# Optimization experiments

Hardware: AMD Instinct MI355X
Metric: run time of the kernel (lower is better)

Reference implementation:

```python
import jax, jax.numpy as jnp
import numpy as np

NUM_HEADS = 16
BLOCK = 64  # block_size = min(64, N)

def setup_inputs() -> dict:
    key = jax.random.key(0)
    k0, k1, k2 = jax.random.split(key, 3)
    B, N, C = 2, 2048, 1024
    x = jax.random.normal(k0, (B, N, C), dtype=jnp.float32)
    w_qkv = jax.random.normal(k1, (3 * C, C), dtype=jnp.float32) * 0.02  # torch Linear weight [out,in]
    w_proj = jax.random.normal(k2, (C, C), dtype=jnp.float32) * 0.02
    b_proj = jnp.zeros((C,), dtype=jnp.float32)
    return {"x": x, "w_qkv": w_qkv, "w_proj": w_proj, "b_proj": b_proj}

def reference(x, w_qkv, w_proj, b_proj):
    B, N, C = x.shape
    H = NUM_HEADS
    hd = C // H
    bs = min(BLOCK, N)
    scale = hd ** -0.5
    # qkv projection: [B,N,3C] -> [3,B,H,N,hd]
    qkv = (x @ w_qkv.T).reshape(B, N, 3, H, hd).transpose(2, 0, 3, 1, 4)
    q, k, v = qkv[0], qkv[1], qkv[2]
    # block-causal mask: query block i attends to all key blocks <= i
    blk = jnp.arange(N) // bs
    mask = blk[:, None] >= blk[None, :]  # [N,N]
    scores = jnp.einsum('bhqd,bhkd->bhqk', q, k) * scale
    scores = jnp.where(mask, scores, -jnp.inf)
    weights = jax.nn.softmax(scores, axis=-1)
    out = jnp.einsum('bhqk,bhkd->bhqd', weights, v)
    out = out.transpose(0, 2, 1, 3).reshape(B, N, C)
    return out @ w_proj.T + b_proj
```

## Files before the change

### kernel.cpp

```cpp
#include <hip/hip_runtime.h>

typedef __attribute__((ext_vector_type(8))) short bf16x8;
typedef __attribute__((ext_vector_type(4))) float f32x4;
typedef __attribute__((ext_vector_type(2))) unsigned int u32x2;

__device__ __forceinline__ unsigned short f2bf(float f) {
  unsigned int u = __float_as_uint(f);
  u += 0x7fffu + ((u >> 16) & 1u);
  return (unsigned short)(u >> 16);
}

__device__ __forceinline__ void gload_lds16(const unsigned short* g, unsigned short* l) {
  __builtin_amdgcn_global_load_lds(
      (const __attribute__((address_space(1))) unsigned int*)g,
      (__attribute__((address_space(3))) unsigned int*)l,
      16, 0, 0);
}

__global__ void cvt_all(const float* __restrict__ x, const float* __restrict__ wq,
                        const float* __restrict__ wp, unsigned short* __restrict__ dst) {
  const int n1 = 4096 * 1024 / 4, n2 = 3072 * 1024 / 4, n3 = 1024 * 1024 / 4;
  int stride = gridDim.x * blockDim.x;
  for (int i = blockIdx.x * blockDim.x + threadIdx.x; i < n1 + n2 + n3; i += stride) {
    const float* s; int j;
    if (i < n1)           { s = x;  j = i; }
    else if (i < n1 + n2) { s = wq; j = i - n1; }
    else                  { s = wp; j = i - n1 - n2; }
    float4 v = ((const float4*)s)[j];
    ushort4 o;
    o.x = f2bf(v.x); o.y = f2bf(v.y); o.z = f2bf(v.z); o.w = f2bf(v.w);
    ((ushort4*)dst)[i] = o;
  }
}

__device__ __forceinline__ void gemm128_bt(const unsigned short* __restrict__ A,
                                           const unsigned short* __restrict__ Bt,
                                           unsigned short* As, unsigned short* Bs,
                                           int tm, int tn, f32x4 acc[4][4]) {
  const int K = 1024;
  int tid = threadIdx.x;
  int w = tid >> 6, l = tid & 63;
  int wr = w >> 1, wc = w & 1;
  int g = l >> 4, c = l & 15;

  int srow = w * 32 + (l >> 2);
  int skoff = (((l & 3) ^ ((srow >> 1) & 3)) * 8);
  const unsigned short* gA = A + (size_t)(tm * 128 + srow) * K + skoff;
  const unsigned short* gB = Bt + (size_t)(tn * 128 + srow) * K + skoff;
  unsigned short* lA = As + (w * 32) * 32;
  unsigned short* lB = Bs + (w * 32) * 32;

  int rx = (c >> 1) & 3;
  int arow = wr * 64 + c;
  int brow = wc * 64 + c;

  for (int k0 = 0; k0 < K; k0 += 32) {
    gload_lds16(gA, lA);
    gload_lds16(gA + 16 * K, lA + 16 * 32);
    gload_lds16(gB, lB);
    gload_lds16(gB + 16 * K, lB + 16 * 32);
    gA += 32; gB += 32;
    __syncthreads();
    bf16x8 af[4], bfr[4];
#pragma unroll
    for (int mi = 0; mi < 4; ++mi)
      af[mi] = *(const bf16x8*)((const char*)As + (arow + mi * 16) * 64 + ((g ^ rx) << 4));
#pragma unroll
    for (int ni = 0; ni < 4; ++ni)
      bfr[ni] = *(const bf16x8*)((const char*)Bs + (brow + ni * 16) * 64 + ((g ^ rx) << 4));
#pragma unroll
    for (int mi = 0; mi < 4; ++mi)
#pragma unroll
      for (int ni = 0; ni < 4; ++ni)
        acc[mi][ni] = __builtin_amdgcn_mfma_f32_16x16x32_bf16(af[mi], bfr[ni], acc[mi][ni], 0, 0, 0);
    __syncthreads();
  }
}

__global__ __launch_bounds__(256) void qkv_gemm(const unsigned short* __restrict__ xb,
                                                const unsigned short* __restrict__ wb,
                                                unsigned short* __restrict__ Qp,
                                                unsigned short* __restrict__ Kp,
                                                unsigned short* __restrict__ Vt) {
  __shared__ unsigned short As[128 * 32];
  __shared__ unsigned short Bs[128 * 32];
  f32x4 acc[4][4];
#pragma unroll
  for (int i = 0; i < 4; ++i)
#pragma unroll
    for (int j = 0; j < 4; ++j) acc[i][j] = f32x4{0.f, 0.f, 0.f, 0.f};
  int id = (blockIdx.x & 7) * 96 + (blockIdx.x >> 3);
  int tm = id / 24, tn = id % 24;
  gemm128_bt(xb, wb, As, Bs, tm, tn, acc);

  int tid = threadIdx.x;
  int w = tid >> 6, l = tid & 63;
  int wr = w >> 1, wc = w & 1;
  int g = l >> 4, c = l & 15;
  const float QSCALE = 0.125f * 1.44269504088896f;
#pragma unroll
  for (int mi = 0; mi < 4; ++mi)
#pragma unroll
    for (int ni = 0; ni < 4; ++ni)
#pragma unroll
      for (int r = 0; r < 4; ++r) {
        int row = tm * 128 + wr * 64 + mi * 16 + g * 4 + r;
        int col = tn * 128 + wc * 64 + ni * 16 + c;
        int b = row >> 11, seq = row & 2047;
        int t = col >> 10;
        int h = (col >> 6) & 15, d = col & 63;
        size_t bh = (size_t)b * 16 + h;
        float v = acc[mi][ni][r];
        if (t == 0)      Qp[(bh * 2048 + seq) * 64 + d] = f2bf(v * QSCALE);
        else if (t == 1) Kp[(bh * 2048 + seq) * 64 + d] = f2bf(v);
        else             Vt[(bh * 64 + d) * 2048 + seq] = f2bf(v);
      }
}

__global__ __launch_bounds__(256, 3) void attn_fa(const unsigned short* __restrict__ Qp,
                                                  const unsigned short* __restrict__ Kp,
                                                  const unsigned short* __restrict__ Vt,
                                                  unsigned short* __restrict__ attn) {
  __shared__ unsigned short Ks[2][4096];
  __shared__ unsigned short Vs[2][4096];
  int tid = threadIdx.x;
  int w = tid >> 6, l = tid & 63;
  int g = l >> 4, c = l & 15;

  int idx = blockIdx.x;
  int pos = idx >> 3;
  int qb = 31 - (pos >> 2);
  int bh = (idx & 7) + 8 * (pos & 3);

  const unsigned short* Qbh = Qp + (size_t)bh * 2048 * 64;
  const unsigned short* Kbh = Kp + (size_t)bh * 2048 * 64;
  const unsigned short* Vbh = Vt + (size_t)bh * 64 * 2048;

  int rowA, colA, rowB, colB;
  { int L = tid * 16;         int P = L ^ (((L >> 7) & 7) << 4); rowA = P >> 7; colA = (P & 127) >> 1; }
  { int L = (tid + 256) * 16; int P = L ^ (((L >> 7) & 7) << 4); rowB = P >> 7; colB = (P & 127) >> 1; }
  const unsigned short* gKA = Kbh + rowA * 64 + colA;
  const unsigned short* gKB = Kbh + rowB * 64 + colB;
  const unsigned short* gVA = Vbh + (size_t)rowA * 2048 + colA;
  const unsigned short* gVB = Vbh + (size_t)rowB * 2048 + colB;

#define STAGE(buf, kb)                                              \
  do {                                                              \
    gload_lds16(gKA + (kb) * 4096, &Ks[(buf)][w * 512]);            \
    gload_lds16(gKB + (kb) * 4096, &Ks[(buf)][w * 512 + 2048]);     \
    gload_lds16(gVA + (kb) * 64,  &Vs[(buf)][w * 512]);             \
    gload_lds16(gVB + (kb) * 64,  &Vs[(buf)][w * 512 + 2048]);      \
  } while (0)

  bf16x8 qf[2];
  {
    size_t qrow = (size_t)qb * 64 + w * 16 + c;
    qf[0] = *(const bf16x8*)(Qbh + qrow * 64 + 8 * g);
    qf[1] = *(const bf16x8*)(Qbh + qrow * 64 + 32 + 8 * g);
  }

  float lp4[4] = {0.f, 0.f, 0.f, 0.f};
  f32x4 o[4];
#pragma unroll
  for (int df = 0; df < 4; ++df) o[df] = f32x4{0.f, 0.f, 0.f, 0.f};

  int xorv = c & 7;

  int cur = 0;
  STAGE(0, 0);
  __syncthreads();
  for (int kb = 0; kb <= qb; ++kb) {
    if (kb < qb) STAGE(1 - cur, kb + 1);

    const char* Kb = (const char*)&Ks[cur][0];
    const char* Vb = (const char*)&Vs[cur][0];
    bf16x8 kf[8];
#pragma unroll
    for (int nf = 0; nf < 4; ++nf) {
      int r = nf * 16 + c;
#pragma unroll
      for (int ks = 0; ks < 2; ++ks)
        kf[nf * 2 + ks] = *(const bf16x8*)(Kb + r * 128 + (((ks * 4 + g) ^ xorv) * 16));
    }
    f32x4 s4[4];
#pragma unroll
    for (int nf = 0; nf < 4; ++nf) {
      s4[nf] = f32x4{0.f, 0.f, 0.f, 0.f};
      s4[nf] = __builtin_amdgcn_mfma_f32_16x16x32_bf16(kf[nf * 2 + 0], qf[0], s4[nf], 0, 0, 0);
      s4[nf] = __builtin_amdgcn_mfma_f32_16x16x32_bf16(kf[nf * 2 + 1], qf[1], s4[nf], 0, 0, 0);
    }
    u32x2 pa[4];
#pragma unroll
    for (int nf = 0; nf < 4; ++nf) {
      float p0 = __builtin_amdgcn_exp2f(s4[nf][0]);
      float p1 = __builtin_amdgcn_exp2f(s4[nf][1]);
      float p2 = __builtin_amdgcn_exp2f(s4[nf][2]);
      float p3 = __builtin_amdgcn_exp2f(s4[nf][3]);
      lp4[nf] += (p0 + p1) + (p2 + p3);
      unsigned int w0, w1;
      asm("v_cvt_pk_bf16_f32 %0, %1, %2" : "=v"(w0) : "v"(p0), "v"(p1));
      asm("v_cvt_pk_bf16_f32 %0, %1, %2" : "=v"(w1) : "v"(p2), "v"(p3));
      pa[nf][0] = w0; pa[nf][1] = w1;
    }
#pragma unroll
    for (int df = 0; df < 4; ++df) {
      int vrow = df * 16 + c;
#pragma unroll
      for (int ks = 0; ks < 4; ++ks) {
        u32x2 vbf = *(const u32x2*)(Vb + vrow * 128 + (((2 * ks + (g >> 1)) ^ xorv) * 16) + 8 * (g & 1));
        asm("v_mfma_f32_16x16x16_bf16 %0, %1, %2, %0"
            : "+v"(o[df]) : "v"(pa[ks]), "v"(vbf));
      }
    }
    __syncthreads();
    cur ^= 1;
  }
#undef STAGE

  float lp = (lp4[0] + lp4[1]) + (lp4[2] + lp4[3]);
  lp += __shfl_xor(lp, 16);
  lp += __shfl_xor(lp, 32);
  float inv[4];
#pragma unroll
  for (int r = 0; r < 4; ++r) inv[r] = __builtin_amdgcn_rcpf(__shfl(lp, g * 4 + r));

  int b = bh >> 4, h = bh & 15;
#pragma unroll
  for (int df = 0; df < 4; ++df)
#pragma unroll
    for (int r = 0; r < 4; ++r) {
      int row = qb * 64 + w * 16 + g * 4 + r;
      int colc = h * 64 + df * 16 + c;
      attn[((size_t)b * 2048 + row) * 1024 + colc] = f2bf(o[df][r] * inv[r]);
    }
}

__global__ __launch_bounds__(256) void proj_gemm(const unsigned short* __restrict__ attn,
                                                 const unsigned short* __restrict__ wpb,
                                                 const float* __restrict__ bias,
                                                 float* __restrict__ out) {
  __shared__ unsigned short As[128 * 32];
  __shared__ unsigned short Bs[128 * 32];
  f32x4 acc[4][4];
#pragma unroll
  for (int i = 0; i < 4; ++i)
#pragma unroll
    for (int j = 0; j < 4; ++j) acc[i][j] = f32x4{0.f, 0.f, 0.f, 0.f};
  int id = (blockIdx.x & 7) * 32 + (blockIdx.x >> 3);
  int tm = id / 8, tn = id % 8;
  gemm128_bt(attn, wpb, As, Bs, tm, tn, acc);

  int tid = threadIdx.x;
  int w = tid >> 6, l = tid & 63;
  int wr = w >> 1, wc = w & 1;
  int g = l >> 4, c = l & 15;
#pragma unroll
  for (int mi = 0; mi < 4; ++mi)
#pragma unroll
    for (int ni = 0; ni < 4; ++ni)
#pragma unroll
      for (int r = 0; r < 4; ++r) {
        int row = tm * 128 + wr * 64 + mi * 16 + g * 4 + r;
        int col = tn * 128 + wc * 64 + ni * 16 + c;
        out[(size_t)row * 1024 + col] = acc[mi][ni][r] + bias[col];
      }
}

extern "C" void kernel_launch(void* const* d_in, const int* in_sizes, int n_in,
                              void* d_out, int out_size, void* d_ws, size_t ws_size,
                              hipStream_t stream) {
  (void)in_sizes; (void)n_in; (void)out_size; (void)ws_size;
  const float* x      = (const float*)d_in[0];
  const float* w_qkv  = (const float*)d_in[1];
  const float* w_proj = (const float*)d_in[2];
  const float* b_proj = (const float*)d_in[3];
  float* out = (float*)d_out;

  unsigned short* xb    = (unsigned short*)d_ws;
  unsigned short* wqkvb = xb + 4096 * 1024;
  unsigned short* wpb   = wqkvb + 3072 * 1024;
  unsigned short* Qp    = wpb + 1024 * 1024;
  unsigned short* Kp    = Qp + 32 * 2048 * 64;
  unsigned short* Vt    = Kp + 32 * 2048 * 64;
  unsigned short* attn  = Vt + 32 * 64 * 2048;

  cvt_all<<<2048, 256, 0, stream>>>(x, w_qkv, w_proj, xb);
  qkv_gemm<<<768, 256, 0, stream>>>(xb, wqkvb, Qp, Kp, Vt);
  attn_fa<<<1024, 256, 0, stream>>>(Qp, Kp, Vt, attn);
  proj_gemm<<<256, 256, 0, stream>>>(attn, wpb, b_proj, out);
}
```

Before: 110.0 us.

## Load V fragments directly from global memory and widen conversion kernel vectors

The attention kernel no longer stages V tiles through shared memory. Each lane now reads its V fragments for the PV MMA straight from global memory at the start of each key block. This halves LDS usage and raises the occupancy hint from 3 to 4 blocks per SM. The cost is more uncoalesced 8-byte global loads on the critical path, with no double buffering to hide them. Separately, the fp32-to-bf16 conversion kernel now handles 8 elements per thread with 16-byte stores and is launched with half as many blocks.

```diff
diff --git a/kernel.cpp b/kernel.cpp
--- a/kernel.cpp
+++ b/kernel.cpp
@@ -3,6 +3,7 @@
 typedef __attribute__((ext_vector_type(8))) short bf16x8;
 typedef __attribute__((ext_vector_type(4))) float f32x4;
 typedef __attribute__((ext_vector_type(2))) unsigned int u32x2;
+typedef __attribute__((ext_vector_type(8))) unsigned short ushort8v;
 
 __device__ __forceinline__ unsigned short f2bf(float f) {
   unsigned int u = __float_as_uint(f);
@@ -19,17 +20,19 @@
 
 __global__ void cvt_all(const float* __restrict__ x, const float* __restrict__ wq,
                         const float* __restrict__ wp, unsigned short* __restrict__ dst) {
-  const int n1 = 4096 * 1024 / 4, n2 = 3072 * 1024 / 4, n3 = 1024 * 1024 / 4;
+  const int n1 = 4096 * 1024 / 8, n2 = 3072 * 1024 / 8, n3 = 1024 * 1024 / 8;
   int stride = gridDim.x * blockDim.x;
   for (int i = blockIdx.x * blockDim.x + threadIdx.x; i < n1 + n2 + n3; i += stride) {
     const float* s; int j;
     if (i < n1)           { s = x;  j = i; }
     else if (i < n1 + n2) { s = wq; j = i - n1; }
     else                  { s = wp; j = i - n1 - n2; }
-    float4 v = ((const float4*)s)[j];
-    ushort4 o;
-    o.x = f2bf(v.x); o.y = f2bf(v.y); o.z = f2bf(v.z); o.w = f2bf(v.w);
-    ((ushort4*)dst)[i] = o;
+    float4 a = ((const float4*)s)[j * 2];
+    float4 b = ((const float4*)s)[j * 2 + 1];
+    ushort8v o;
+    o[0] = f2bf(a.x); o[1] = f2bf(a.y); o[2] = f2bf(a.z); o[3] = f2bf(a.w);
+    o[4] = f2bf(b.x); o[5] = f2bf(b.y); o[6] = f2bf(b.z); o[7] = f2bf(b.w);
+    ((ushort8v*)dst)[i] = o;
   }
 }
 
@@ -117,12 +120,11 @@
       }
 }
 
-__global__ __launch_bounds__(256, 3) void attn_fa(const unsigned short* __restrict__ Qp,
+__global__ __launch_bounds__(256, 4) void attn_fa(const unsigned short* __restrict__ Qp,
                                                   const unsigned short* __restrict__ Kp,
                                                   const unsigned short* __restrict__ Vt,
                                                   unsigned short* __restrict__ attn) {
   __shared__ unsigned short Ks[2][4096];
-  __shared__ unsigned short Vs[2][4096];
   int tid = threadIdx.x;
   int w = tid >> 6, l = tid & 63;
   int g = l >> 4, c = l & 15;
@@ -141,15 +143,11 @@
   { int L = (tid + 256) * 16; int P = L ^ (((L >> 7) & 7) << 4); rowB = P >> 7; colB = (P & 127) >> 1; }
   const unsigned short* gKA = Kbh + rowA * 64 + colA;
   const unsigned short* gKB = Kbh + rowB * 64 + colB;
-  const unsigned short* gVA = Vbh + (size_t)rowA * 2048 + colA;
-  const unsigned short* gVB = Vbh + (size_t)rowB * 2048 + colB;
 
 #define STAGE(buf, kb)                                              \
   do {                                                              \
     gload_lds16(gKA + (kb) * 4096, &Ks[(buf)][w * 512]);            \
     gload_lds16(gKB + (kb) * 4096, &Ks[(buf)][w * 512 + 2048]);     \
-    gload_lds16(gVA + (kb) * 64,  &Vs[(buf)][w * 512]);             \
-    gload_lds16(gVB + (kb) * 64,  &Vs[(buf)][w * 512 + 2048]);      \
   } while (0)
 
   bf16x8 qf[2];
@@ -158,6 +156,7 @@
     qf[0] = *(const bf16x8*)(Qbh + qrow * 64 + 8 * g);
     qf[1] = *(const bf16x8*)(Qbh + qrow * 64 + 32 + 8 * g);
   }
+  const unsigned short* Vlane = Vbh + (size_t)c * 2048 + 4 * g;
 
   float lp4[4] = {0.f, 0.f, 0.f, 0.f};
   f32x4 o[4];
@@ -172,8 +171,14 @@
   for (int kb = 0; kb <= qb; ++kb) {
     if (kb < qb) STAGE(1 - cur, kb + 1);
 
+    u32x2 vf[4][4];
+#pragma unroll
+    for (int df = 0; df < 4; ++df)
+#pragma unroll
+      for (int ks = 0; ks < 4; ++ks)
+        vf[df][ks] = *(const u32x2*)(Vlane + (size_t)df * 16 * 2048 + kb * 64 + ks * 16);
+
     const char* Kb = (const char*)&Ks[cur][0];
-    const char* Vb = (const char*)&Vs[cur][0];
     bf16x8 kf[8];
 #pragma unroll
     for (int nf = 0; nf < 4; ++nf) {
@@ -203,15 +208,11 @@
       pa[nf][0] = w0; pa[nf][1] = w1;
     }
 #pragma unroll
-    for (int df = 0; df < 4; ++df) {
-      int vrow = df * 16 + c;
-#pragma unroll
-      for (int ks = 0; ks < 4; ++ks) {
-        u32x2 vbf = *(const u32x2*)(Vb + vrow * 128 + (((2 * ks + (g >> 1)) ^ xorv) * 16) + 8 * (g & 1));
+    for (int df = 0; df < 4; ++df)
+#pragma unroll
+      for (int ks = 0; ks < 4; ++ks)
         asm("v_mfma_f32_16x16x16_bf16 %0, %1, %2, %0"
-            : "+v"(o[df]) : "v"(pa[ks]), "v"(vbf));
-      }
-    }
+            : "+v"(o[df]) : "v"(pa[ks]), "v"(vf[df][ks]));
     __syncthreads();
     cur ^= 1;
   }
@@ -284,7 +285,7 @@
   unsigned short* Vt    = Kp + 32 * 2048 * 64;
   unsigned short* attn  = Vt + 32 * 64 * 2048;
 
-  cvt_all<<<2048, 256, 0, stream>>>(x, w_qkv, w_proj, xb);
+  cvt_all<<<1024, 256, 0, stream>>>(x, w_qkv, w_proj, xb);
   qkv_gemm<<<768, 256, 0, stream>>>(xb, wqkvb, Qp, Kp, Vt);
   attn_fa<<<1024, 256, 0, stream>>>(Qp, Kp, Vt, attn);
   proj_gemm<<<256, 256, 0, stream>>>(attn, wpb, b_proj, out);
```

After: 221.6 us. +101.3%, slower.

## Process two query blocks per attention workgroup to reuse K/V tiles

Applied to the files above, without the earlier changes.

Each attention workgroup now handles a pair of adjacent 64-row query blocks (2p, 2p+1). Each K/V tile loaded into LDS is then shared by both blocks, which roughly halves global K/V traffic and the staging and barrier overhead per query block. The launch grid drops from 1024 to 512 workgroups, with register pressure higher from the doubled accumulators and fewer waves available to fill the GPU. Separately, the bf16 conversion kernel now handles 8 elements per thread with 16-byte stores and uses half as many blocks.

```diff
diff --git a/kernel.cpp b/kernel.cpp
--- a/kernel.cpp
+++ b/kernel.cpp
@@ -3,6 +3,7 @@
 typedef __attribute__((ext_vector_type(8))) short bf16x8;
 typedef __attribute__((ext_vector_type(4))) float f32x4;
 typedef __attribute__((ext_vector_type(2))) unsigned int u32x2;
+typedef __attribute__((ext_vector_type(8))) unsigned short ushort8v;
 
 __device__ __forceinline__ unsigned short f2bf(float f) {
   unsigned int u = __float_as_uint(f);
@@ -19,17 +20,19 @@
 
 __global__ void cvt_all(const float* __restrict__ x, const float* __restrict__ wq,
                         const float* __restrict__ wp, unsigned short* __restrict__ dst) {
-  const int n1 = 4096 * 1024 / 4, n2 = 3072 * 1024 / 4, n3 = 1024 * 1024 / 4;
+  const int n1 = 4096 * 1024 / 8, n2 = 3072 * 1024 / 8, n3 = 1024 * 1024 / 8;
   int stride = gridDim.x * blockDim.x;
   for (int i = blockIdx.x * blockDim.x + threadIdx.x; i < n1 + n2 + n3; i += stride) {
     const float* s; int j;
     if (i < n1)           { s = x;  j = i; }
     else if (i < n1 + n2) { s = wq; j = i - n1; }
     else                  { s = wp; j = i - n1 - n2; }
-    float4 v = ((const float4*)s)[j];
-    ushort4 o;
-    o.x = f2bf(v.x); o.y = f2bf(v.y); o.z = f2bf(v.z); o.w = f2bf(v.w);
-    ((ushort4*)dst)[i] = o;
+    float4 a = ((const float4*)s)[j * 2];
+    float4 b = ((const float4*)s)[j * 2 + 1];
+    ushort8v o;
+    o[0] = f2bf(a.x); o[1] = f2bf(a.y); o[2] = f2bf(a.z); o[3] = f2bf(a.w);
+    o[4] = f2bf(b.x); o[5] = f2bf(b.y); o[6] = f2bf(b.z); o[7] = f2bf(b.w);
+    ((ushort8v*)dst)[i] = o;
   }
 }
 
@@ -129,8 +132,9 @@
 
   int idx = blockIdx.x;
   int pos = idx >> 3;
-  int qb = 31 - (pos >> 2);
+  int p = 15 - (pos >> 2);
   int bh = (idx & 7) + 8 * (pos & 3);
+  int qlo = 2 * p, qhi = 2 * p + 1;
 
   const unsigned short* Qbh = Qp + (size_t)bh * 2048 * 64;
   const unsigned short* Kbh = Kp + (size_t)bh * 2048 * 64;
@@ -152,25 +156,30 @@
     gload_lds16(gVB + (kb) * 64,  &Vs[(buf)][w * 512 + 2048]);      \
   } while (0)
 
-  bf16x8 qf[2];
+  bf16x8 qfl[2], qfh[2];
   {
-    size_t qrow = (size_t)qb * 64 + w * 16 + c;
-    qf[0] = *(const bf16x8*)(Qbh + qrow * 64 + 8 * g);
-    qf[1] = *(const bf16x8*)(Qbh + qrow * 64 + 32 + 8 * g);
-  }
-
-  float lp4[4] = {0.f, 0.f, 0.f, 0.f};
-  f32x4 o[4];
-#pragma unroll
-  for (int df = 0; df < 4; ++df) o[df] = f32x4{0.f, 0.f, 0.f, 0.f};
+    size_t qr0 = (size_t)qlo * 64 + w * 16 + c;
+    size_t qr1 = (size_t)qhi * 64 + w * 16 + c;
+    qfl[0] = *(const bf16x8*)(Qbh + qr0 * 64 + 8 * g);
+    qfl[1] = *(const bf16x8*)(Qbh + qr0 * 64 + 32 + 8 * g);
+    qfh[0] = *(const bf16x8*)(Qbh + qr1 * 64 + 8 * g);
+    qfh[1] = *(const bf16x8*)(Qbh + qr1 * 64 + 32 + 8 * g);
+  }
+
+  float lpl[4] = {0.f, 0.f, 0.f, 0.f}, lph[4] = {0.f, 0.f, 0.f, 0.f};
+  f32x4 ol[4], oh[4];
+#pragma unroll
+  for (int df = 0; df < 4; ++df) { ol[df] = f32x4{0.f, 0.f, 0.f, 0.f}; oh[df] = f32x4{0.f, 0.f, 0.f, 0.f}; }
 
   int xorv = c & 7;
 
   int cur = 0;
   STAGE(0, 0);
   __syncthreads();
-  for (int kb = 0; kb <= qb; ++kb) {
-    if (kb < qb) STAGE(1 - cur, kb + 1);
+  int last = qhi;
+  for (int kb = 0; kb <= last; ++kb) {
+    if (kb < last) STAGE(1 - cur, kb + 1);
+    bool do_lo = (kb <= qlo);
 
     const char* Kb = (const char*)&Ks[cur][0];
     const char* Vb = (const char*)&Vs[cur][0];
@@ -182,25 +191,47 @@
       for (int ks = 0; ks < 2; ++ks)
         kf[nf * 2 + ks] = *(const bf16x8*)(Kb + r * 128 + (((ks * 4 + g) ^ xorv) * 16));
     }
-    f32x4 s4[4];
+    f32x4 sl[4], sh[4];
 #pragma unroll
     for (int nf = 0; nf < 4; ++nf) {
-      s4[nf] = f32x4{0.f, 0.f, 0.f, 0.f};
-      s4[nf] = __builtin_amdgcn_mfma_f32_16x16x32_bf16(kf[nf * 2 + 0], qf[0], s4[nf], 0, 0, 0);
-      s4[nf] = __builtin_amdgcn_mfma_f32_16x16x32_bf16(kf[nf * 2 + 1], qf[1], s4[nf], 0, 0, 0);
-    }
-    u32x2 pa[4];
+      sh[nf] = f32x4{0.f, 0.f, 0.f, 0.f};
+      sh[nf] = __builtin_amdgcn_mfma_f32_16x16x32_bf16(kf[nf * 2 + 0], qfh[0], sh[nf], 0, 0, 0);
+      sh[nf] = __builtin_amdgcn_mfma_f32_16x16x32_bf16(kf[nf * 2 + 1], qfh[1], sh[nf], 0, 0, 0);
+    }
+    if (do_lo) {
+#pragma unroll
+      for (int nf = 0; nf < 4; ++nf) {
+        sl[nf] = f32x4{0.f, 0.f, 0.f, 0.f};
+        sl[nf] = __builtin_amdgcn_mfma_f32_16x16x32_bf16(kf[nf * 2 + 0], qfl[0], sl[nf], 0, 0, 0);
+        sl[nf] = __builtin_amdgcn_mfma_f32_16x16x32_bf16(kf[nf * 2 + 1], qfl[1], sl[nf], 0, 0, 0);
+      }
+    }
+    u32x2 pal[4], pah[4];
 #pragma unroll
     for (int nf = 0; nf < 4; ++nf) {
-      float p0 = __builtin_amdgcn_exp2f(s4[nf][0]);
-      float p1 = __builtin_amdgcn_exp2f(s4[nf][1]);
-      float p2 = __builtin_amdgcn_exp2f(s4[nf][2]);
-      float p3 = __builtin_amdgcn_exp2f(s4[nf][3]);
-      lp4[nf] += (p0 + p1) + (p2 + p3);
+      float p0 = __builtin_amdgcn_exp2f(sh[nf][0]);
+      float p1 = __builtin_amdgcn_exp2f(sh[nf][1]);
+      float p2 = __builtin_amdgcn_exp2f(sh[nf][2]);
+      float p3 = __builtin_amdgcn_exp2f(sh[nf][3]);
+      lph[nf] += (p0 + p1) + (p2 + p3);
       unsigned int w0, w1;
       asm("v_cvt_pk_bf16_f32 %0, %1, %2" : "=v"(w0) : "v"(p0), "v"(p1));
       asm("v_cvt_pk_bf16_f32 %0, %1, %2" : "=v"(w1) : "v"(p2), "v"(p3));
-      pa[nf][0] = w0; pa[nf][1] = w1;
+      pah[nf][0] = w0; pah[nf][1] = w1;
+    }
+    if (do_lo) {
+#pragma unroll
+      for (int nf = 0; nf < 4; ++nf) {
+        float p0 = __builtin_amdgcn_exp2f(sl[nf][0]);
+        float p1 = __builtin_amdgcn_exp2f(sl[nf][1]);
+        float p2 = __builtin_amdgcn_exp2f(sl[nf][2]);
+        float p3 = __builtin_amdgcn_exp2f(sl[nf][3]);
+        lpl[nf] += (p0 + p1) + (p2 + p3);
+        unsigned int w0, w1;
+        asm("v_cvt_pk_bf16_f32 %0, %1, %2" : "=v"(w0) : "v"(p0), "v"(p1));
+        asm("v_cvt_pk_bf16_f32 %0, %1, %2" : "=v"(w1) : "v"(p2), "v"(p3));
+        pal[nf][0] = w0; pal[nf][1] = w1;
+      }
     }
 #pragma unroll
     for (int df = 0; df < 4; ++df) {
@@ -208,8 +239,9 @@
 #pragma unroll
       for (int ks = 0; ks < 4; ++ks) {
         u32x2 vbf = *(const u32x2*)(Vb + vrow * 128 + (((2 * ks + (g >> 1)) ^ xorv) * 16) + 8 * (g & 1));
-        asm("v_mfma_f32_16x16x16_bf16 %0, %1, %2, %0"
-            : "+v"(o[df]) : "v"(pa[ks]), "v"(vbf));
+        asm("v_mfma_f32_16x16x16_bf16 %0, %1, %2, %0" : "+v"(oh[df]) : "v"(pah[ks]), "v"(vbf));
+        if (do_lo)
+          asm("v_mfma_f32_16x16x16_bf16 %0, %1, %2, %0" : "+v"(ol[df]) : "v"(pal[ks]), "v"(vbf));
       }
     }
     __syncthreads();
@@ -217,21 +249,27 @@
   }
 #undef STAGE
 
-  float lp = (lp4[0] + lp4[1]) + (lp4[2] + lp4[3]);
-  lp += __shfl_xor(lp, 16);
-  lp += __shfl_xor(lp, 32);
-  float inv[4];
-#pragma unroll
-  for (int r = 0; r < 4; ++r) inv[r] = __builtin_amdgcn_rcpf(__shfl(lp, g * 4 + r));
+  float sl2 = (lpl[0] + lpl[1]) + (lpl[2] + lpl[3]);
+  float sh2 = (lph[0] + lph[1]) + (lph[2] + lph[3]);
+  sl2 += __shfl_xor(sl2, 16); sl2 += __shfl_xor(sl2, 32);
+  sh2 += __shfl_xor(sh2, 16); sh2 += __shfl_xor(sh2, 32);
+  float invl[4], invh[4];
+#pragma unroll
+  for (int r = 0; r < 4; ++r) {
+    invl[r] = __builtin_amdgcn_rcpf(__shfl(sl2, g * 4 + r));
+    invh[r] = __builtin_amdgcn_rcpf(__shfl(sh2, g * 4 + r));
+  }
 
   int b = bh >> 4, h = bh & 15;
 #pragma unroll
   for (int df = 0; df < 4; ++df)
 #pragma unroll
     for (int r = 0; r < 4; ++r) {
-      int row = qb * 64 + w * 16 + g * 4 + r;
       int colc = h * 64 + df * 16 + c;
-      attn[((size_t)b * 2048 + row) * 1024 + colc] = f2bf(o[df][r] * inv[r]);
+      int rl = qlo * 64 + w * 16 + g * 4 + r;
+      int rh = qhi * 64 + w * 16 + g * 4 + r;
+      attn[((size_t)b * 2048 + rl) * 1024 + colc] = f2bf(ol[df][r] * invl[r]);
+      attn[((size_t)b * 2048 + rh) * 1024 + colc] = f2bf(oh[df][r] * invh[r]);
     }
 }
 
@@ -284,8 +322,8 @@
   unsigned short* Vt    = Kp + 32 * 2048 * 64;
   unsigned short* attn  = Vt + 32 * 64 * 2048;
 
-  cvt_all<<<2048, 256, 0, stream>>>(x, w_qkv, w_proj, xb);
+  cvt_all<<<1024, 256, 0, stream>>>(x, w_qkv, w_proj, xb);
   qkv_gemm<<<768, 256, 0, stream>>>(xb, wqkvb, Qp, Kp, Vt);
-  attn_fa<<<1024, 256, 0, stream>>>(Qp, Kp, Vt, attn);
+  attn_fa<<<512, 256, 0, stream>>>(Qp, Kp, Vt, attn);
   proj_gemm<<<256, 256, 0, stream>>>(attn, wpb, b_proj, out);
 }
```

Result: slower. 122.5 us (+11.3%).

## Double-buffer GEMM LDS staging and widen fp32-to-bf16 conversion to 8 elements

Applied to the files above, without the earlier changes.

The shared GEMM mainloop now uses two LDS buffers, so the next K-tile is prefetched with global_load_lds while MFMAs run on the current one, and one barrier per iteration is removed. This is meant to hide global-load latency in the qkv and projection GEMMs, at the cost of doubling their LDS use, which may reduce occupancy. The conversion kernel also handles 8 floats per thread with 16-byte stores and a halved grid. One caveat: there is no explicit wait on the async LDS loads before the barrier, so correctness depends on how the compiler inserts vmcnt waits.

```diff
diff --git a/kernel.cpp b/kernel.cpp
--- a/kernel.cpp
+++ b/kernel.cpp
@@ -3,6 +3,7 @@
 typedef __attribute__((ext_vector_type(8))) short bf16x8;
 typedef __attribute__((ext_vector_type(4))) float f32x4;
 typedef __attribute__((ext_vector_type(2))) unsigned int u32x2;
+typedef __attribute__((ext_vector_type(8))) unsigned short ushort8v;
 
 __device__ __forceinline__ unsigned short f2bf(float f) {
   unsigned int u = __float_as_uint(f);
@@ -19,17 +20,19 @@
 
 __global__ void cvt_all(const float* __restrict__ x, const float* __restrict__ wq,
                         const float* __restrict__ wp, unsigned short* __restrict__ dst) {
-  const int n1 = 4096 * 1024 / 4, n2 = 3072 * 1024 / 4, n3 = 1024 * 1024 / 4;
+  const int n1 = 4096 * 1024 / 8, n2 = 3072 * 1024 / 8, n3 = 1024 * 1024 / 8;
   int stride = gridDim.x * blockDim.x;
   for (int i = blockIdx.x * blockDim.x + threadIdx.x; i < n1 + n2 + n3; i += stride) {
     const float* s; int j;
     if (i < n1)           { s = x;  j = i; }
     else if (i < n1 + n2) { s = wq; j = i - n1; }
     else                  { s = wp; j = i - n1 - n2; }
-    float4 v = ((const float4*)s)[j];
-    ushort4 o;
-    o.x = f2bf(v.x); o.y = f2bf(v.y); o.z = f2bf(v.z); o.w = f2bf(v.w);
-    ((ushort4*)dst)[i] = o;
+    float4 a = ((const float4*)s)[j * 2];
+    float4 b = ((const float4*)s)[j * 2 + 1];
+    ushort8v o;
+    o[0] = f2bf(a.x); o[1] = f2bf(a.y); o[2] = f2bf(a.z); o[3] = f2bf(a.w);
+    o[4] = f2bf(b.x); o[5] = f2bf(b.y); o[6] = f2bf(b.z); o[7] = f2bf(b.w);
+    ((ushort8v*)dst)[i] = o;
   }
 }
 
@@ -54,27 +57,39 @@
   int arow = wr * 64 + c;
   int brow = wc * 64 + c;
 
-  for (int k0 = 0; k0 < K; k0 += 32) {
-    gload_lds16(gA, lA);
-    gload_lds16(gA + 16 * K, lA + 16 * 32);
-    gload_lds16(gB, lB);
-    gload_lds16(gB + 16 * K, lB + 16 * 32);
-    gA += 32; gB += 32;
-    __syncthreads();
+#define STG(buf, t)                                                  \
+  do {                                                               \
+    const unsigned short* ga_ = gA + (t) * 32;                       \
+    const unsigned short* gb_ = gB + (t) * 32;                       \
+    gload_lds16(ga_, lA + (buf) * 4096);                             \
+    gload_lds16(ga_ + 16 * K, lA + (buf) * 4096 + 16 * 32);          \
+    gload_lds16(gb_, lB + (buf) * 4096);                             \
+    gload_lds16(gb_ + 16 * K, lB + (buf) * 4096 + 16 * 32);          \
+  } while (0)
+
+  int cur = 0;
+  STG(0, 0);
+  __syncthreads();
+  for (int t = 0; t < 32; ++t) {
+    if (t + 1 < 32) STG(1 - cur, t + 1);
+    const char* Ab = (const char*)(As + cur * 4096);
+    const char* Bb = (const char*)(Bs + cur * 4096);
     bf16x8 af[4], bfr[4];
 #pragma unroll
     for (int mi = 0; mi < 4; ++mi)
-      af[mi] = *(const bf16x8*)((const char*)As + (arow + mi * 16) * 64 + ((g ^ rx) << 4));
+      af[mi] = *(const bf16x8*)(Ab + (arow + mi * 16) * 64 + ((g ^ rx) << 4));
 #pragma unroll
     for (int ni = 0; ni < 4; ++ni)
-      bfr[ni] = *(const bf16x8*)((const char*)Bs + (brow + ni * 16) * 64 + ((g ^ rx) << 4));
+      bfr[ni] = *(const bf16x8*)(Bb + (brow + ni * 16) * 64 + ((g ^ rx) << 4));
 #pragma unroll
     for (int mi = 0; mi < 4; ++mi)
 #pragma unroll
       for (int ni = 0; ni < 4; ++ni)
         acc[mi][ni] = __builtin_amdgcn_mfma_f32_16x16x32_bf16(af[mi], bfr[ni], acc[mi][ni], 0, 0, 0);
     __syncthreads();
+    cur ^= 1;
   }
+#undef STG
 }
 
 __global__ __launch_bounds__(256) void qkv_gemm(const unsigned short* __restrict__ xb,
@@ -82,8 +97,8 @@
                                                 unsigned short* __restrict__ Qp,
                                                 unsigned short* __restrict__ Kp,
                                                 unsigned short* __restrict__ Vt) {
-  __shared__ unsigned short As[128 * 32];
-  __shared__ unsigned short Bs[128 * 32];
+  __shared__ unsigned short As[2 * 128 * 32];
+  __shared__ unsigned short Bs[2 * 128 * 32];
   f32x4 acc[4][4];
 #pragma unroll
   for (int i = 0; i < 4; ++i)
@@ -239,8 +254,8 @@
                                                  const unsigned short* __restrict__ wpb,
                                                  const float* __restrict__ bias,
                                                  float* __restrict__ out) {
-  __shared__ unsigned short As[128 * 32];
-  __shared__ unsigned short Bs[128 * 32];
+  __shared__ unsigned short As[2 * 128 * 32];
+  __shared__ unsigned short Bs[2 * 128 * 32];
   f32x4 acc[4][4];
 #pragma unroll
   for (int i = 0; i < 4; ++i)
@@ -284,7 +299,7 @@
   unsigned short* Vt    = Kp + 32 * 2048 * 64;
   unsigned short* attn  = Vt + 32 * 64 * 2048;
 
-  cvt_all<<<2048, 256, 0, stream>>>(x, w_qkv, w_proj, xb);
+  cvt_all<<<1024, 256, 0, stream>>>(x, w_qkv, w_proj, xb);
   qkv_gemm<<<768, 256, 0, stream>>>(xb, wqkvb, Qp, Kp, Vt);
   attn_fa<<<1024, 256, 0, stream>>>(Qp, Kp, Vt, attn);
   proj_gemm<<<256, 256, 0, stream>>>(attn, wpb, b_proj, out);
```

After: 120.4 us. +9.4%, slower.
